# Kernel tuning notes

Hardware: AMD Instinct MI355X
Metric: run time of the kernel (lower is better)

Reference implementation:

```python
import math
import jax, jax.numpy as jnp
import numpy as np

S, D, E = 8192, 2048, 64            # tokens, model_dim, num_experts
CAPACITY_FACTOR = 1.0
CAP = int(CAPACITY_FACTOR * math.ceil(S / E))  # 128, static (training-mode 'drop' gate)


def setup_inputs() -> dict:
    key = jax.random.key(0)
    kx, kw = jax.random.split(key)
    x = jax.random.normal(kx, (S, D), dtype=jnp.float32)
    wg = jax.random.normal(kw, (E, D), dtype=jnp.float32) * 0.02  # Linear(D, E, bias=False) weight
    return {"x": x, "wg": wg}


def reference(x, wg):
    # logits = self.wg(input)
    logits = jnp.einsum('sd,ed->se', x, wg)                 # [S, E]
    gates = jax.nn.softmax(logits, axis=1)                  # [S, E]
    indices1_s = jnp.argmax(gates, axis=1)                  # [S]
    mask1 = jax.nn.one_hot(indices1_s, E, dtype=gates.dtype)  # [S, E]

    # load-balancing aux loss
    me = jnp.mean(gates, axis=0)
    ce = jnp.mean(mask1, axis=0)
    l_aux = jnp.mean(me * ce) * (E * E)

    # gates1_s computed BEFORE capacity drop (as in source)
    gates1_s = jnp.sum(gates * mask1, axis=1)               # [S]

    # fused_cumsum_sub_one: position of each token within its expert's queue
    locations1 = jnp.cumsum(mask1, axis=0) - 1.0            # [S, E]
    # capacity drop ('drop' gate type)
    mask1 = mask1 * (locations1 < CAP).astype(mask1.dtype)
    locations1_s = jnp.sum(locations1 * mask1, axis=1).astype(jnp.int32)  # [S]

    gates1 = gates1_s[:, None] * mask1                      # [S, E]
    locations1_sc = jax.nn.one_hot(locations1_s, CAP, dtype=gates1.dtype)  # [S, CAP]
    # bmm(gates1[:,:,None], loc_sc[:,None,:]) == outer product per token
    combine1_sec = jnp.einsum('se,sc->sec', gates1, locations1_sc)  # [S, E, CAP]
    dispatch_mask = combine1_sec.astype(bool)
    return l_aux, combine1_sec, dispatch_mask
```

## Files before the change

kernel.cpp:

```cpp
#include <hip/hip_runtime.h>
#include <cstddef>
#include <cstdint>

#define S_TOK 8192
#define DDIM  2048
#define NEXP  64
#define CAPTY 128
#define KC    64
#define TPB   64
#define NBLK  (S_TOK / TPB)
#define SPLITK 8
#define KPER  (DDIM / SPLITK)
#define SEC   (S_TOK * NEXP * CAPTY)

__global__ __launch_bounds__(256)
void fill_zero_kernel(float* __restrict__ out)
{
    const size_t n4 = (size_t)SEC / 2;
    float4* out4 = (float4*)out;
    size_t i = (size_t)blockIdx.x * 256 + threadIdx.x;
    const size_t stride = (size_t)gridDim.x * 256;
    float4 z = make_float4(0.f, 0.f, 0.f, 0.f);
    for (size_t idx = i; idx < n4; idx += stride)
        out4[idx] = z;
    if (i == 0) out[(size_t)2 * SEC] = 0.0f;
}

__global__ __launch_bounds__(256)
void gate_gemm_kernel(const float* __restrict__ x, const float* __restrict__ wg,
                      float* __restrict__ part)
{
    __shared__ float xs[KC][TPB + 2];
    __shared__ float ws[KC][NEXP];

    const int tid = threadIdx.x;
    const int e4  = tid & 15;
    const int tg  = tid >> 4;
    const int kp  = blockIdx.x & (SPLITK - 1);
    const int tc  = blockIdx.x >> 3;
    const int t_base = tc * TPB;
    const int k_base = kp * KPER;

    float acc[4][4];
#pragma unroll
    for (int i = 0; i < 4; ++i)
#pragma unroll
        for (int j = 0; j < 4; ++j) acc[i][j] = 0.0f;

    for (int kc0 = 0; kc0 < KPER; kc0 += KC) {
        const int kc = k_base + kc0;
        __syncthreads();
#pragma unroll
        for (int m = 0; m < 4; ++m) {
            int idx = tid + 256 * m;
            int t = idx & 63;
            int c = idx >> 6;
            float4 v = *(const float4*)(x + (size_t)(t_base + t) * DDIM + kc + c * 4);
            xs[c * 4 + 0][t] = v.x;
            xs[c * 4 + 1][t] = v.y;
            xs[c * 4 + 2][t] = v.z;
            xs[c * 4 + 3][t] = v.w;
            float4 w = *(const float4*)(wg + (size_t)t * DDIM + kc + c * 4);
            ws[c * 4 + 0][t] = w.x;
            ws[c * 4 + 1][t] = w.y;
            ws[c * 4 + 2][t] = w.z;
            ws[c * 4 + 3][t] = w.w;
        }
        __syncthreads();
#pragma unroll 8
        for (int k = 0; k < KC; ++k) {
            float4 wv = *(const float4*)&ws[k][e4 * 4];
            float2 xa = *(const float2*)&xs[k][tg * 4];
            float2 xb = *(const float2*)&xs[k][tg * 4 + 2];
            float xv0 = xa.x, xv1 = xa.y, xv2 = xb.x, xv3 = xb.y;
            acc[0][0] += xv0 * wv.x; acc[0][1] += xv0 * wv.y;
            acc[0][2] += xv0 * wv.z; acc[0][3] += xv0 * wv.w;
            acc[1][0] += xv1 * wv.x; acc[1][1] += xv1 * wv.y;
            acc[1][2] += xv1 * wv.z; acc[1][3] += xv1 * wv.w;
            acc[2][0] += xv2 * wv.x; acc[2][1] += xv2 * wv.y;
            acc[2][2] += xv2 * wv.z; acc[2][3] += xv2 * wv.w;
            acc[3][0] += xv3 * wv.x; acc[3][1] += xv3 * wv.y;
            acc[3][2] += xv3 * wv.z; acc[3][3] += xv3 * wv.w;
        }
    }

#pragma unroll
    for (int i = 0; i < 4; ++i) {
        float4 v = make_float4(acc[i][0], acc[i][1], acc[i][2], acc[i][3]);
        *(float4*)(part + ((size_t)kp * S_TOK + t_base + tg * 4 + i) * NEXP + e4 * 4) = v;
    }
}

__global__ __launch_bounds__(64)
void softmax_kernel(const float* __restrict__ part,
                    float* __restrict__ gate_s, int* __restrict__ expert,
                    int* __restrict__ rank, int* __restrict__ hist,
                    float* __restrict__ partial_g)
{
    __shared__ float probs[TPB][NEXP + 1];
    __shared__ int   sexp[TPB];

    const int t   = threadIdx.x;
    const int tok = blockIdx.x * TPB + t;

    float lg[NEXP];
#pragma unroll
    for (int e = 0; e < NEXP; e += 4) {
        float4 v = *(const float4*)(part + (size_t)tok * NEXP + e);
        lg[e] = v.x; lg[e + 1] = v.y; lg[e + 2] = v.z; lg[e + 3] = v.w;
    }
#pragma unroll
    for (int kp = 1; kp < SPLITK; ++kp) {
#pragma unroll
        for (int e = 0; e < NEXP; e += 4) {
            float4 v = *(const float4*)(part + ((size_t)kp * S_TOK + tok) * NEXP + e);
            lg[e] += v.x; lg[e + 1] += v.y; lg[e + 2] += v.z; lg[e + 3] += v.w;
        }
    }

    float m = -1e30f; int am = 0;
#pragma unroll
    for (int e = 0; e < NEXP; ++e)
        if (lg[e] > m) { m = lg[e]; am = e; }
    float s = 0.0f;
#pragma unroll
    for (int e = 0; e < NEXP; ++e) { float p = __expf(lg[e] - m); lg[e] = p; s += p; }
    float rcp = 1.0f / s;
#pragma unroll
    for (int e = 0; e < NEXP; ++e) probs[t][e] = lg[e] * rcp;

    sexp[t] = am;
    gate_s[tok] = rcp;
    expert[tok] = am;
    __syncthreads();

    int r = 0;
    for (int u = 0; u < t; ++u) r += (sexp[u] == am) ? 1 : 0;
    rank[tok] = r;

    {
        int e = t;
        float pg = 0.0f; int cnt = 0;
        for (int u = 0; u < TPB; ++u) {
            pg  += probs[u][e];
            cnt += (sexp[u] == e) ? 1 : 0;
        }
        partial_g[blockIdx.x * NEXP + e] = pg;
        hist[blockIdx.x * NEXP + e]      = cnt;
    }
}

__global__ __launch_bounds__(64)
void scan_kernel(const int* __restrict__ hist, const float* __restrict__ partial_g,
                 int* __restrict__ chunk_base, float* __restrict__ out)
{
    int e = threadIdx.x;
    int base = 0;
    float sg = 0.0f;
    for (int c = 0; c < NBLK; ++c) {
        chunk_base[c * NEXP + e] = base;
        base += hist[c * NEXP + e];
        sg   += partial_g[c * NEXP + e];
    }
    float v = sg * (float)base;
#pragma unroll
    for (int off = 32; off > 0; off >>= 1) v += __shfl_down(v, off);
    if (e == 0)
        out[0] = v * (64.0f / (8192.0f * 8192.0f));
}

__global__ __launch_bounds__(256)
void scatter_kernel(const float* __restrict__ gate_s, const int* __restrict__ expert,
                    const int* __restrict__ rank, const int* __restrict__ chunk_base,
                    float* __restrict__ out)
{
    int s = blockIdx.x * 256 + threadIdx.x;
    if (s >= S_TOK) return;
    int e   = expert[s];
    int loc = chunk_base[(s >> 6) * NEXP + e] + rank[s];
    if (loc < CAPTY) {
        size_t idx = 1 + (size_t)s * (NEXP * CAPTY) + (size_t)e * CAPTY + loc;
        out[idx]       = gate_s[s];
        out[idx + SEC] = 1.0f;
    }
}

extern "C" void kernel_launch(void* const* d_in, const int* in_sizes, int n_in,
                              void* d_out, int out_size, void* d_ws, size_t ws_size,
                              hipStream_t stream)
{
    const float* x  = (const float*)d_in[0];
    const float* wg = (const float*)d_in[1];
    float* out = (float*)d_out;
    char* ws = (char*)d_ws;

    float* part      = (float*)(ws + 0);
    size_t off = (size_t)SPLITK * S_TOK * NEXP * sizeof(float);
    float* gate_s    = (float*)(ws + off);          off += 32768;
    int*   expert    = (int*)  (ws + off);          off += 32768;
    int*   rank      = (int*)  (ws + off);          off += 32768;
    int*   hist      = (int*)  (ws + off);          off += 32768;
    int*   chunk_b   = (int*)  (ws + off);          off += 32768;
    float* partial_g = (float*)(ws + off);

    fill_zero_kernel<<<4096, 256, 0, stream>>>(out);
    gate_gemm_kernel<<<NBLK * SPLITK, 256, 0, stream>>>(x, wg, part);
    softmax_kernel<<<NBLK, 64, 0, stream>>>(part, gate_s, expert, rank, hist, partial_g);
    scan_kernel<<<1, 64, 0, stream>>>(hist, partial_g, chunk_b, out);
    scatter_kernel<<<(S_TOK + 255) / 256, 256, 0, stream>>>(gate_s, expert, rank, chunk_b, out);
}
```

Baseline: 630.8 us.

## Replace zero-fill kernel with memset and restructure gate GEMM and softmax

Drops the custom float4 zero-fill kernel and clears the large output with hipMemsetAsync placed just before the scatter, moving l_aux through a workspace slot so the memset does not overwrite it. The gate GEMM now stores x row-major in shared memory with vectorized loads and a k-by-4 register-blocked inner loop. The softmax kernel uses 256 threads so the split-K reduction is spread across four threads per token. The memset may or may not reach the bandwidth of the custom fill, and it depends on out_size being in float elements.

```diff
diff --git a/kernel.cpp b/kernel.cpp
--- a/kernel.cpp
+++ b/kernel.cpp
@@ -11,30 +11,17 @@
 #define NBLK  (S_TOK / TPB)
 #define SPLITK 8
 #define KPER  (DDIM / SPLITK)
-#define SEC   (S_TOK * NEXP * CAPTY)
-
-__global__ __launch_bounds__(256)
-void fill_zero_kernel(float* __restrict__ out)
-{
-    const size_t n4 = (size_t)SEC / 2;
-    float4* out4 = (float4*)out;
-    size_t i = (size_t)blockIdx.x * 256 + threadIdx.x;
-    const size_t stride = (size_t)gridDim.x * 256;
-    float4 z = make_float4(0.f, 0.f, 0.f, 0.f);
-    for (size_t idx = i; idx < n4; idx += stride)
-        out4[idx] = z;
-    if (i == 0) out[(size_t)2 * SEC] = 0.0f;
-}
+#define SEC   ((size_t)S_TOK * NEXP * CAPTY)
 
 __global__ __launch_bounds__(256)
 void gate_gemm_kernel(const float* __restrict__ x, const float* __restrict__ wg,
                       float* __restrict__ part)
 {
-    __shared__ float xs[KC][TPB + 2];
+    __shared__ float xs[TPB][72];
     __shared__ float ws[KC][NEXP];
 
     const int tid = threadIdx.x;
-    const int e4  = tid & 15;
+    const int el  = tid & 15;
     const int tg  = tid >> 4;
     const int kp  = blockIdx.x & (SPLITK - 1);
     const int tc  = blockIdx.x >> 3;
@@ -53,45 +40,56 @@
 #pragma unroll
         for (int m = 0; m < 4; ++m) {
             int idx = tid + 256 * m;
-            int t = idx & 63;
+            int t = idx >> 4;
+            int c = idx & 15;
+            float4 v = *(const float4*)(x + (size_t)(t_base + t) * DDIM + kc + c * 4);
+            *(float4*)&xs[t][c * 4] = v;
+        }
+#pragma unroll
+        for (int m = 0; m < 4; ++m) {
+            int idx = tid + 256 * m;
+            int e = idx & 63;
             int c = idx >> 6;
-            float4 v = *(const float4*)(x + (size_t)(t_base + t) * DDIM + kc + c * 4);
-            xs[c * 4 + 0][t] = v.x;
-            xs[c * 4 + 1][t] = v.y;
-            xs[c * 4 + 2][t] = v.z;
-            xs[c * 4 + 3][t] = v.w;
-            float4 w = *(const float4*)(wg + (size_t)t * DDIM + kc + c * 4);
-            ws[c * 4 + 0][t] = w.x;
-            ws[c * 4 + 1][t] = w.y;
-            ws[c * 4 + 2][t] = w.z;
-            ws[c * 4 + 3][t] = w.w;
+            float4 w = *(const float4*)(wg + (size_t)e * DDIM + kc + c * 4);
+            ws[c * 4 + 0][e] = w.x;
+            ws[c * 4 + 1][e] = w.y;
+            ws[c * 4 + 2][e] = w.z;
+            ws[c * 4 + 3][e] = w.w;
         }
         __syncthreads();
-#pragma unroll 8
-        for (int k = 0; k < KC; ++k) {
-            float4 wv = *(const float4*)&ws[k][e4 * 4];
-            float2 xa = *(const float2*)&xs[k][tg * 4];
-            float2 xb = *(const float2*)&xs[k][tg * 4 + 2];
-            float xv0 = xa.x, xv1 = xa.y, xv2 = xb.x, xv3 = xb.y;
-            acc[0][0] += xv0 * wv.x; acc[0][1] += xv0 * wv.y;
-            acc[0][2] += xv0 * wv.z; acc[0][3] += xv0 * wv.w;
-            acc[1][0] += xv1 * wv.x; acc[1][1] += xv1 * wv.y;
-            acc[1][2] += xv1 * wv.z; acc[1][3] += xv1 * wv.w;
-            acc[2][0] += xv2 * wv.x; acc[2][1] += xv2 * wv.y;
-            acc[2][2] += xv2 * wv.z; acc[2][3] += xv2 * wv.w;
-            acc[3][0] += xv3 * wv.x; acc[3][1] += xv3 * wv.y;
-            acc[3][2] += xv3 * wv.z; acc[3][3] += xv3 * wv.w;
+
+#pragma unroll
+        for (int k4 = 0; k4 < KC; k4 += 4) {
+            float4 xv[4], wv[4];
+#pragma unroll
+            for (int i = 0; i < 4; ++i)
+                xv[i] = *(const float4*)&xs[tg + 16 * i][k4];
+#pragma unroll
+            for (int j = 0; j < 4; ++j)
+                wv[j] = *(const float4*)&ws[k4 + j][el * 4];
+#pragma unroll
+            for (int i = 0; i < 4; ++i) {
+                acc[i][0] += xv[i].x * wv[0].x; acc[i][1] += xv[i].x * wv[0].y;
+                acc[i][2] += xv[i].x * wv[0].z; acc[i][3] += xv[i].x * wv[0].w;
+                acc[i][0] += xv[i].y * wv[1].x; acc[i][1] += xv[i].y * wv[1].y;
+                acc[i][2] += xv[i].y * wv[1].z; acc[i][3] += xv[i].y * wv[1].w;
+                acc[i][0] += xv[i].z * wv[2].x; acc[i][1] += xv[i].z * wv[2].y;
+                acc[i][2] += xv[i].z * wv[2].z; acc[i][3] += xv[i].z * wv[2].w;
+                acc[i][0] += xv[i].w * wv[3].x; acc[i][1] += xv[i].w * wv[3].y;
+                acc[i][2] += xv[i].w * wv[3].z; acc[i][3] += xv[i].w * wv[3].w;
+            }
         }
     }
 
 #pragma unroll
     for (int i = 0; i < 4; ++i) {
+        int t = tg + 16 * i;
         float4 v = make_float4(acc[i][0], acc[i][1], acc[i][2], acc[i][3]);
-        *(float4*)(part + ((size_t)kp * S_TOK + t_base + tg * 4 + i) * NEXP + e4 * 4) = v;
-    }
-}
-
-__global__ __launch_bounds__(64)
+        *(float4*)(part + ((size_t)kp * S_TOK + t_base + t) * NEXP + el * 4) = v;
+    }
+}
+
+__global__ __launch_bounds__(256)
 void softmax_kernel(const float* __restrict__ part,
                     float* __restrict__ gate_s, int* __restrict__ expert,
                     int* __restrict__ rank, int* __restrict__ hist,
@@ -100,46 +98,52 @@
     __shared__ float probs[TPB][NEXP + 1];
     __shared__ int   sexp[TPB];
 
-    const int t   = threadIdx.x;
-    const int tok = blockIdx.x * TPB + t;
-
-    float lg[NEXP];
-#pragma unroll
-    for (int e = 0; e < NEXP; e += 4) {
-        float4 v = *(const float4*)(part + (size_t)tok * NEXP + e);
-        lg[e] = v.x; lg[e + 1] = v.y; lg[e + 2] = v.z; lg[e + 3] = v.w;
-    }
-#pragma unroll
-    for (int kp = 1; kp < SPLITK; ++kp) {
-#pragma unroll
-        for (int e = 0; e < NEXP; e += 4) {
-            float4 v = *(const float4*)(part + ((size_t)kp * S_TOK + tok) * NEXP + e);
-            lg[e] += v.x; lg[e + 1] += v.y; lg[e + 2] += v.z; lg[e + 3] += v.w;
-        }
-    }
-
-    float m = -1e30f; int am = 0;
-#pragma unroll
-    for (int e = 0; e < NEXP; ++e)
-        if (lg[e] > m) { m = lg[e]; am = e; }
-    float s = 0.0f;
-#pragma unroll
-    for (int e = 0; e < NEXP; ++e) { float p = __expf(lg[e] - m); lg[e] = p; s += p; }
-    float rcp = 1.0f / s;
-#pragma unroll
-    for (int e = 0; e < NEXP; ++e) probs[t][e] = lg[e] * rcp;
-
-    sexp[t] = am;
-    gate_s[tok] = rcp;
-    expert[tok] = am;
+    const int tid = threadIdx.x;
+    const int t_base = blockIdx.x * TPB;
+    const int t = tid >> 2, q = tid & 3;
+    const int tok = t_base + t;
+
+#pragma unroll
+    for (int jj = 0; jj < 4; ++jj) {
+        float4 a = make_float4(0.f, 0.f, 0.f, 0.f);
+#pragma unroll
+        for (int kpp = 0; kpp < SPLITK; ++kpp) {
+            float4 v = *(const float4*)(part + ((size_t)kpp * S_TOK + tok) * NEXP + q * 16 + jj * 4);
+            a.x += v.x; a.y += v.y; a.z += v.z; a.w += v.w;
+        }
+        probs[t][q * 16 + jj * 4 + 0] = a.x;
+        probs[t][q * 16 + jj * 4 + 1] = a.y;
+        probs[t][q * 16 + jj * 4 + 2] = a.z;
+        probs[t][q * 16 + jj * 4 + 3] = a.w;
+    }
     __syncthreads();
 
-    int r = 0;
-    for (int u = 0; u < t; ++u) r += (sexp[u] == am) ? 1 : 0;
-    rank[tok] = r;
-
-    {
-        int e = t;
+    if (tid < TPB) {
+        const int t2 = tid, tok2 = t_base + t2;
+        float m = -1e30f; int am = 0;
+        for (int e = 0; e < NEXP; ++e) {
+            float v = probs[t2][e];
+            if (v > m) { m = v; am = e; }
+        }
+        float s = 0.0f;
+        for (int e = 0; e < NEXP; ++e) s += __expf(probs[t2][e] - m);
+        float rcp = 1.0f / s;
+        for (int e = 0; e < NEXP; ++e)
+            probs[t2][e] = __expf(probs[t2][e] - m) * rcp;
+        sexp[t2] = am;
+        gate_s[tok2] = rcp;
+        expert[tok2] = am;
+    }
+    __syncthreads();
+
+    if (tid < TPB) {
+        const int t2 = tid;
+        const int am = sexp[t2];
+        int r = 0;
+        for (int u = 0; u < t2; ++u) r += (sexp[u] == am) ? 1 : 0;
+        rank[t_base + t2] = r;
+    } else if (tid < 2 * TPB) {
+        const int e = tid - TPB;
         float pg = 0.0f; int cnt = 0;
         for (int u = 0; u < TPB; ++u) {
             pg  += probs[u][e];
@@ -152,7 +156,7 @@
 
 __global__ __launch_bounds__(64)
 void scan_kernel(const int* __restrict__ hist, const float* __restrict__ partial_g,
-                 int* __restrict__ chunk_base, float* __restrict__ out)
+                 int* __restrict__ chunk_base, float* __restrict__ l_aux_ws)
 {
     int e = threadIdx.x;
     int base = 0;
@@ -166,15 +170,16 @@
 #pragma unroll
     for (int off = 32; off > 0; off >>= 1) v += __shfl_down(v, off);
     if (e == 0)
-        out[0] = v * (64.0f / (8192.0f * 8192.0f));
+        l_aux_ws[0] = v * (64.0f / (8192.0f * 8192.0f));
 }
 
 __global__ __launch_bounds__(256)
 void scatter_kernel(const float* __restrict__ gate_s, const int* __restrict__ expert,
                     const int* __restrict__ rank, const int* __restrict__ chunk_base,
-                    float* __restrict__ out)
+                    const float* __restrict__ l_aux_ws, float* __restrict__ out)
 {
     int s = blockIdx.x * 256 + threadIdx.x;
+    if (s == 0) out[0] = l_aux_ws[0];
     if (s >= S_TOK) return;
     int e   = expert[s];
     int loc = chunk_base[(s >> 6) * NEXP + e] + rank[s];
@@ -200,12 +205,14 @@
     int*   expert    = (int*)  (ws + off);          off += 32768;
     int*   rank      = (int*)  (ws + off);          off += 32768;
     int*   hist      = (int*)  (ws + off);          off += 32768;
+    float* partial_g = (float*)(ws + off);          off += 32768;
     int*   chunk_b   = (int*)  (ws + off);          off += 32768;
-    float* partial_g = (float*)(ws + off);
-
-    fill_zero_kernel<<<4096, 256, 0, stream>>>(out);
+    float* l_aux_ws  = (float*)(ws + off);
+
     gate_gemm_kernel<<<NBLK * SPLITK, 256, 0, stream>>>(x, wg, part);
-    softmax_kernel<<<NBLK, 64, 0, stream>>>(part, gate_s, expert, rank, hist, partial_g);
-    scan_kernel<<<1, 64, 0, stream>>>(hist, partial_g, chunk_b, out);
-    scatter_kernel<<<(S_TOK + 255) / 256, 256, 0, stream>>>(gate_s, expert, rank, chunk_b, out);
-}
+    softmax_kernel<<<NBLK, 256, 0, stream>>>(part, gate_s, expert, rank, hist, partial_g);
+    scan_kernel<<<1, 64, 0, stream>>>(hist, partial_g, chunk_b, l_aux_ws);
+    hipMemsetAsync(d_out, 0, (size_t)out_size * sizeof(float), stream);
+    scatter_kernel<<<(S_TOK + 255) / 256, 256, 0, stream>>>(gate_s, expert, rank,
+                                                            chunk_b, l_aux_ws, out);
+}
```

Measured after the change: 595.5 us. 1.06x faster.
